# Optimization experiments

Hardware: AMD Instinct MI355X
Metric: run time of the kernel (lower is better)

Reference implementation:

```python
import jax, jax.numpy as jnp
import numpy as np

N = 100_000      # nodes
E = 1_600_000    # edges
D_IN = 256       # input feature dim
H, C = 4, 32     # heads, per-head channels (out_channels=32)
D_OUT = H * C    # 128
EPS = 1e-5


def setup_inputs() -> dict:
    key = jax.random.key(0)
    ks = jax.random.split(key, 8)
    f = jnp.float32
    return {
        "x": jax.random.normal(ks[0], (N, D_IN), f),
        "edge_index": jax.random.randint(ks[1], (2, E), 0, N, dtype=jnp.int32),
        "Wq": jax.random.normal(ks[2], (D_IN, D_OUT), f) * 0.05,
        "bq": jnp.zeros((D_OUT,), f),
        "Wk": jax.random.normal(ks[3], (D_IN, D_OUT), f) * 0.05,
        "bk": jnp.zeros((D_OUT,), f),
        "Wv": jax.random.normal(ks[4], (D_IN, D_OUT), f) * 0.05,
        "bv": jnp.zeros((D_OUT,), f),
        "Wskip": jax.random.normal(ks[5], (D_IN, D_OUT), f) * 0.05,
        "bskip": jnp.zeros((D_OUT,), f),
        "gn_weight": jnp.ones((D_OUT,), f),
        "gn_bias": jnp.zeros((D_OUT,), f),
        "gn_mean_scale": jnp.ones((D_OUT,), f),
    }


def reference(x, edge_index, Wq, bq, Wk, bk, Wv, bv, Wskip, bskip,
              gn_weight, gn_bias, gn_mean_scale):
    n = x.shape[0]
    src, dst = edge_index[0], edge_index[1]  # message flows src -> dst

    # ---- TransformerConv (heads=4, concat=True, root_weight=True) ----
    q = (x @ Wq + bq).reshape(n, H, C)
    k = (x @ Wk + bk).reshape(n, H, C)
    v = (x @ Wv + bv).reshape(n, H, C)

    # per-edge attention logits [E, H]
    score = jnp.einsum("ehc,ehc->eh", q[dst], k[src]) / jnp.sqrt(jnp.float32(C))

    # segment softmax over incoming edges of each destination node
    m = jax.ops.segment_max(score, dst, num_segments=n)        # [N, H]
    e = jnp.exp(score - m[dst])                                # [E, H]
    denom = jax.ops.segment_sum(e, dst, num_segments=n)        # [N, H]
    alpha = e / denom[dst]                                     # [E, H]

    # weighted aggregation of values: [E, H, C] -> [N, H, C]
    msg = alpha[:, :, None] * v[src]
    out = jax.ops.segment_sum(msg, dst, num_segments=n).reshape(n, D_OUT)

    # root (skip) transform
    out = out + x @ Wskip + bskip

    # ---- GraphNorm (single graph) ----
    mean = out.mean(axis=0)                                    # [D_OUT]
    centered = out - mean * gn_mean_scale
    var = (centered * centered).mean(axis=0)
    out = gn_weight * centered * jax.lax.rsqrt(var + EPS) + gn_bias

    # ---- Mish ----
    return out * jnp.tanh(jax.nn.softplus(out))
```

## Files before the change

### kernel.cpp

```cpp
#include <hip/hip_runtime.h>
#include <hip/hip_bf16.h>
#include <math.h>

#define N_NODES 100000
#define N_EDGES 1600000
#define D_IN    256
#define D_OUT   128
#define NHEAD   4
#define CH      32
#define GN_EPS  1e-5f

typedef __attribute__((ext_vector_type(8))) short bf16x8;
typedef __attribute__((ext_vector_type(4))) float f32x4;

__device__ inline float bf2f(unsigned short u) {
    return __uint_as_float(((unsigned int)u) << 16);
}
__device__ inline unsigned short f2bf(float f) {
    unsigned int x = __float_as_uint(f);
    unsigned int r = (x + 0x7fffu + ((x >> 16) & 1u)) >> 16;
    return (unsigned short)r;
}
__device__ inline unsigned int pk2bf(float a, float b) {
    __hip_bfloat162 h = __float22bfloat162_rn(float2{a, b});
    return *(unsigned int*)&h;
}
__device__ inline float mishf(float x) {
    if (x > 15.0f) return x;
    float ex = __expf(x);
    float t = ex * (ex + 2.0f);
    return x * t / (t + 2.0f);
}
__device__ inline void gload_lds16(const void* g, void* l) {
    __builtin_amdgcn_global_load_lds(
        (const __attribute__((address_space(1))) unsigned int*)g,
        (__attribute__((address_space(3))) unsigned int*)l,
        16, 0, 0);
}

__global__ void prep_w(const float* __restrict__ Wq, const float* __restrict__ Wk,
                       const float* __restrict__ Wv, const float* __restrict__ Wsk,
                       const float* __restrict__ bq, const float* __restrict__ bk,
                       const float* __restrict__ bv, const float* __restrict__ bsk,
                       unsigned short* __restrict__ Wt2, float* __restrict__ bcat) {
    int idx = blockIdx.x * 256 + threadIdx.x;
    int k   = idx >> 9;
    int col = idx & 511;
    int which = col >> 7, c = col & 127;
    const float* W = (which == 0) ? Wq : (which == 1) ? Wk : (which == 2) ? Wv : Wsk;
    int ks = k >> 5, cc = (k >> 3) & 3, j = k & 7;
    int p = cc ^ ((col >> 2) & 3);
    Wt2[(size_t)ks * 16384 + col * 32 + p * 8 + j] = f2bf(W[(size_t)k * 128 + c]);
    if (idx < 512) {
        int w2 = idx >> 7, c2 = idx & 127;
        const float* b = (w2 == 0) ? bq : (w2 == 1) ? bk : (w2 == 2) ? bv : bsk;
        bcat[idx] = b[c2];
    }
}

__global__ __launch_bounds__(512, 4) void gemm_mfma(
    const float* __restrict__ x, const unsigned short* __restrict__ Wt2,
    const float* __restrict__ bcat,
    unsigned short* __restrict__ qb, unsigned short* __restrict__ kb,
    unsigned short* __restrict__ vb, float* __restrict__ skip)
{
    __shared__ unsigned short as_[2][64 * 32];
    __shared__ unsigned short bs_[2][512 * 32];
    const int tid = threadIdx.x;
    const int nb = blockIdx.x * 64;

    const int wave = tid >> 6, lane = tid & 63;
    const int lm = lane & 15, lk = lane >> 4;
    const int wr = wave >> 2, wc = wave & 3;

    const int srow = tid >> 3;
    const int sk4  = (tid & 7) * 4;
    float4 areg;

    auto loadA = [&](int ks) {
        areg = make_float4(0.f, 0.f, 0.f, 0.f);
        int grow = nb + srow;
        if (grow < N_NODES)
            areg = *(const float4*)(x + (size_t)grow * D_IN + ks * 32 + sk4);
    };
    auto writeA = [&](int pb) {
        int cc = sk4 >> 3;
        int p = cc ^ ((srow >> 2) & 3);
        uint2 w;
        w.x = pk2bf(areg.x, areg.y);
        w.y = pk2bf(areg.z, areg.w);
        *(uint2*)(as_[pb] + srow * 32 + p * 8 + (sk4 & 7)) = w;
    };
    auto stageB = [&](int ks, int pb) {
        const unsigned short* g = Wt2 + (size_t)ks * 16384;
        #pragma unroll
        for (int it = 0; it < 4; ++it) {
            int u = it * 512 + tid;
            gload_lds16(g + u * 8, bs_[pb] + u * 8);
        }
    };

    f32x4 acc[2][8] = {};

    stageB(0, 0);
    loadA(0);
    writeA(0);
    __syncthreads();

    for (int ks = 0; ks < 8; ++ks) {
        const int pb = ks & 1;
        if (ks < 7) {
            stageB(ks + 1, pb ^ 1);
            loadA(ks + 1);
        }

        bf16x8 a[2], b[8];
        #pragma unroll
        for (int rf = 0; rf < 2; ++rf) {
            int row = wr * 32 + rf * 16 + lm;
            int p = lk ^ ((row >> 2) & 3);
            a[rf] = *(const bf16x8*)(as_[pb] + row * 32 + p * 8);
        }
        #pragma unroll
        for (int cf = 0; cf < 8; ++cf) {
            int col = wc * 128 + cf * 16 + lm;
            int p = lk ^ ((col >> 2) & 3);
            b[cf] = *(const bf16x8*)(bs_[pb] + col * 32 + p * 8);
        }
        #pragma unroll
        for (int cf = 0; cf < 8; ++cf) {
            acc[0][cf] = __builtin_amdgcn_mfma_f32_16x16x32_bf16(a[0], b[cf], acc[0][cf], 0, 0, 0);
            acc[1][cf] = __builtin_amdgcn_mfma_f32_16x16x32_bf16(a[1], b[cf], acc[1][cf], 0, 0, 0);
        }

        if (ks < 7) writeA(pb ^ 1);
        __syncthreads();
    }

    unsigned short* dstb = (wc == 0) ? qb : (wc == 1) ? kb : vb;
    const float* biasp = bcat + wc * 128;
    #pragma unroll
    for (int rf = 0; rf < 2; ++rf) {
        #pragma unroll
        for (int j = 0; j < 4; ++j) {
            const int r = nb + wr * 32 + rf * 16 + lk * 4 + j;
            if (r < N_NODES) {
                if (wc == 3) {
                    #pragma unroll
                    for (int cf = 0; cf < 8; ++cf) {
                        const int col = cf * 16 + lm;
                        skip[(size_t)r * D_OUT + col] = acc[rf][cf][j] + biasp[col];
                    }
                } else {
                    #pragma unroll
                    for (int cf = 0; cf < 8; ++cf) {
                        const int col = cf * 16 + lm;
                        dstb[(size_t)r * D_OUT + col] = f2bf(acc[rf][cf][j] + biasp[col]);
                    }
                }
            }
        }
    }
}

__global__ void hist_kernel(const int* __restrict__ dst, int* __restrict__ deg) {
    int e = blockIdx.x * 256 + threadIdx.x;
    if (e < N_EDGES) atomicAdd(&deg[dst[e]], 1);
}

__global__ __launch_bounds__(256) void scan1(const int* __restrict__ deg,
                                             int* __restrict__ off,
                                             int* __restrict__ bsum) {
    __shared__ int lds[256];
    int t = threadIdx.x;
    int base = blockIdx.x * 1024 + t * 4;
    int d0 = 0, d1 = 0, d2 = 0, d3 = 0;
    if (base + 3 < N_NODES) {
        int4 dd = *(const int4*)(deg + base);
        d0 = dd.x; d1 = dd.y; d2 = dd.z; d3 = dd.w;
    } else {
        if (base     < N_NODES) d0 = deg[base];
        if (base + 1 < N_NODES) d1 = deg[base + 1];
        if (base + 2 < N_NODES) d2 = deg[base + 2];
        if (base + 3 < N_NODES) d3 = deg[base + 3];
    }
    int s = d0 + d1 + d2 + d3;
    lds[t] = s;
    __syncthreads();
    for (int d = 1; d < 256; d <<= 1) {
        int u = (t >= d) ? lds[t - d] : 0;
        __syncthreads();
        lds[t] += u;
        __syncthreads();
    }
    int excl = lds[t] - s;
    if (base     < N_NODES) off[base]     = excl;
    if (base + 1 < N_NODES) off[base + 1] = excl + d0;
    if (base + 2 < N_NODES) off[base + 2] = excl + d0 + d1;
    if (base + 3 < N_NODES) off[base + 3] = excl + d0 + d1 + d2;
    if (t == 255) bsum[blockIdx.x] = lds[255];
}

__global__ void scan2(int* __restrict__ bsum) {
    __shared__ int lds[128];
    int t = threadIdx.x;
    int v = (t < 98) ? bsum[t] : 0;
    lds[t] = v;
    __syncthreads();
    for (int d = 1; d < 128; d <<= 1) {
        int u = (t >= d) ? lds[t - d] : 0;
        __syncthreads();
        lds[t] += u;
        __syncthreads();
    }
    if (t < 98) bsum[t] = lds[t] - v;
}

__global__ void scan3(int* __restrict__ off, int* __restrict__ cursor,
                      const int* __restrict__ bsum) {
    int add = bsum[blockIdx.x];
    int base = blockIdx.x * 1024 + threadIdx.x * 4;
    #pragma unroll
    for (int j = 0; j < 4; ++j) {
        int idx = base + j;
        if (idx < N_NODES) {
            int vv = off[idx] + add;
            off[idx] = vv;
            cursor[idx] = vv;
        }
    }
}

__global__ void scatter_kernel(const int* __restrict__ src, const int* __restrict__ dst,
                               int* __restrict__ cursor, int* __restrict__ ssrc) {
    int e = blockIdx.x * 256 + threadIdx.x;
    if (e < N_EDGES) {
        int d = dst[e];
        int p = atomicAdd(&cursor[d], 1);
        ssrc[p] = src[e];
    }
}

__global__ __launch_bounds__(256) void aggregate(
    const unsigned short* __restrict__ qb, const unsigned short* __restrict__ kb,
    const unsigned short* __restrict__ vb,
    const int* __restrict__ off, const int* __restrict__ endp,
    const int* __restrict__ ssrc, float* __restrict__ out)
{
    const int wave = threadIdx.x >> 6;
    const int lane = threadIdx.x & 63;
    const int n = blockIdx.x * 4 + wave;
    const int c0 = lane * 2;
    const float scale = 0.17677669529663687f;

    unsigned int qv = *(const unsigned int*)(qb + (size_t)n * D_OUT + c0);
    float q0 = bf2f((unsigned short)(qv & 0xffffu));
    float q1 = bf2f((unsigned short)(qv >> 16));

    const int s0 = off[n], s1 = endp[n];

    float m = -1e30f, den = 0.f, a0 = 0.f, a1 = 0.f;

    int i = s0;
    for (; i + 8 <= s1; i += 8) {
        int s[8]; unsigned int kw[8], vw[8]; float p[8], w[8];
        #pragma unroll
        for (int u = 0; u < 8; ++u) s[u] = ssrc[i + u];
        #pragma unroll
        for (int u = 0; u < 8; ++u) kw[u] = *(const unsigned int*)(kb + (size_t)s[u] * D_OUT + c0);
        #pragma unroll
        for (int u = 0; u < 8; ++u) vw[u] = *(const unsigned int*)(vb + (size_t)s[u] * D_OUT + c0);
        #pragma unroll
        for (int u = 0; u < 8; ++u)
            p[u] = q0 * bf2f((unsigned short)(kw[u] & 0xffffu)) + q1 * bf2f((unsigned short)(kw[u] >> 16));
        #pragma unroll
        for (int u = 0; u < 8; ++u) {
            p[u] += __shfl_xor(p[u], 1);
            p[u] += __shfl_xor(p[u], 2);
            p[u] += __shfl_xor(p[u], 4);
            p[u] += __shfl_xor(p[u], 8);
            p[u] *= scale;
        }
        float pm = fmaxf(fmaxf(fmaxf(p[0], p[1]), fmaxf(p[2], p[3])),
                         fmaxf(fmaxf(p[4], p[5]), fmaxf(p[6], p[7])));
        float newm = fmaxf(m, pm);
        float corr = __expf(m - newm);
        float dsum = 0.f, s0a = 0.f, s1a = 0.f;
        #pragma unroll
        for (int u = 0; u < 8; ++u) {
            w[u] = __expf(p[u] - newm);
            dsum += w[u];
            s0a += w[u] * bf2f((unsigned short)(vw[u] & 0xffffu));
            s1a += w[u] * bf2f((unsigned short)(vw[u] >> 16));
        }
        den = den * corr + dsum;
        a0  = a0 * corr + s0a;
        a1  = a1 * corr + s1a;
        m = newm;
    }
    for (; i + 4 <= s1; i += 4) {
        int s[4]; unsigned int kw[4], vw[4]; float p[4], w[4];
        #pragma unroll
        for (int u = 0; u < 4; ++u) s[u] = ssrc[i + u];
        #pragma unroll
        for (int u = 0; u < 4; ++u) kw[u] = *(const unsigned int*)(kb + (size_t)s[u] * D_OUT + c0);
        #pragma unroll
        for (int u = 0; u < 4; ++u) vw[u] = *(const unsigned int*)(vb + (size_t)s[u] * D_OUT + c0);
        #pragma unroll
        for (int u = 0; u < 4; ++u)
            p[u] = q0 * bf2f((unsigned short)(kw[u] & 0xffffu)) + q1 * bf2f((unsigned short)(kw[u] >> 16));
        #pragma unroll
        for (int u = 0; u < 4; ++u) {
            p[u] += __shfl_xor(p[u], 1);
            p[u] += __shfl_xor(p[u], 2);
            p[u] += __shfl_xor(p[u], 4);
            p[u] += __shfl_xor(p[u], 8);
            p[u] *= scale;
        }
        float pm = fmaxf(fmaxf(p[0], p[1]), fmaxf(p[2], p[3]));
        float newm = fmaxf(m, pm);
        float corr = __expf(m - newm);
        float dsum = 0.f, s0a = 0.f, s1a = 0.f;
        #pragma unroll
        for (int u = 0; u < 4; ++u) {
            w[u] = __expf(p[u] - newm);
            dsum += w[u];
            s0a += w[u] * bf2f((unsigned short)(vw[u] & 0xffffu));
            s1a += w[u] * bf2f((unsigned short)(vw[u] >> 16));
        }
        den = den * corr + dsum;
        a0  = a0 * corr + s0a;
        a1  = a1 * corr + s1a;
        m = newm;
    }
    for (; i < s1; ++i) {
        int s = ssrc[i];
        unsigned int kv = *(const unsigned int*)(kb + (size_t)s * D_OUT + c0);
        unsigned int vv = *(const unsigned int*)(vb + (size_t)s * D_OUT + c0);
        float p = q0 * bf2f((unsigned short)(kv & 0xffffu)) + q1 * bf2f((unsigned short)(kv >> 16));
        p += __shfl_xor(p, 1);
        p += __shfl_xor(p, 2);
        p += __shfl_xor(p, 4);
        p += __shfl_xor(p, 8);
        p *= scale;
        float newm = fmaxf(m, p);
        float corr = __expf(m - newm);
        float w = __expf(p - newm);
        den = den * corr + w;
        a0 = a0 * corr + w * bf2f((unsigned short)(vv & 0xffffu));
        a1 = a1 * corr + w * bf2f((unsigned short)(vv >> 16));
        m = newm;
    }

    float invd = (den > 0.f) ? 1.0f / den : 0.f;
    size_t o = (size_t)n * D_OUT + c0;
    float2 sk = *(float2*)(out + o);
    sk.x += a0 * invd;
    sk.y += a1 * invd;
    *(float2*)(out + o) = sk;
}

__global__ __launch_bounds__(256) void norm_reduce(const float* __restrict__ out,
                                                   float* __restrict__ sums) {
    const int total = N_NODES * D_OUT;
    const int stride = gridDim.x * 256;
    int t = threadIdx.x;
    float s = 0.f, s2 = 0.f;
    for (int i = blockIdx.x * 256 + t; i < total; i += stride) {
        float v = out[i];
        s += v; s2 += v * v;
    }
    __shared__ float ls[256], lq[256];
    ls[t] = s; lq[t] = s2;
    __syncthreads();
    if (t < 128) {
        s  = ls[t] + ls[t + 128];
        s2 = lq[t] + lq[t + 128];
        atomicAdd(&sums[t], s);
        atomicAdd(&sums[128 + t], s2);
    }
}

__global__ void finalize(const float* __restrict__ sums, const float* __restrict__ gw,
                         const float* __restrict__ gb, const float* __restrict__ gms,
                         float* __restrict__ AB) {
    int c = threadIdx.x;
    const float invN = 1.0f / (float)N_NODES;
    float mean = sums[c] * invN;
    float ex2  = sums[128 + c] * invN;
    float mu = mean * gms[c];
    float var = ex2 - 2.f * mu * mean + mu * mu;
    float inv = rsqrtf(var + GN_EPS);
    float A = gw[c] * inv;
    AB[c] = A;
    AB[128 + c] = gb[c] - mu * A;
}

__global__ __launch_bounds__(256) void mish_kernel(float* __restrict__ out,
                                                   const float* __restrict__ AB) {
    int i = blockIdx.x * 256 + threadIdx.x;
    int c4 = (i << 2) & 127;
    float4 a  = *(const float4*)(AB + c4);
    float4 b  = *(const float4*)(AB + 128 + c4);
    float4 v  = *(float4*)(out + (size_t)i * 4);
    v.x = mishf(a.x * v.x + b.x);
    v.y = mishf(a.y * v.y + b.y);
    v.z = mishf(a.z * v.z + b.z);
    v.w = mishf(a.w * v.w + b.w);
    *(float4*)(out + (size_t)i * 4) = v;
}

extern "C" void kernel_launch(void* const* d_in, const int* in_sizes, int n_in,
                              void* d_out, int out_size, void* d_ws, size_t ws_size,
                              hipStream_t stream) {
    (void)in_sizes; (void)n_in; (void)out_size; (void)ws_size;

    const float* x    = (const float*)d_in[0];
    const int*   ei   = (const int*)d_in[1];
    const float* Wq   = (const float*)d_in[2];
    const float* bq   = (const float*)d_in[3];
    const float* Wk   = (const float*)d_in[4];
    const float* bk   = (const float*)d_in[5];
    const float* Wv   = (const float*)d_in[6];
    const float* bv   = (const float*)d_in[7];
    const float* Wsk  = (const float*)d_in[8];
    const float* bsk  = (const float*)d_in[9];
    const float* gw   = (const float*)d_in[10];
    const float* gb   = (const float*)d_in[11];
    const float* gms  = (const float*)d_in[12];
    float* out = (float*)d_out;

    char* ws = (char*)d_ws;
    size_t o = 0;
    auto alloc = [&](size_t bytes) -> char* {
        char* p = ws + o;
        o += (bytes + 255) & ~(size_t)255;
        return p;
    };

    unsigned short* qb = (unsigned short*)alloc((size_t)N_NODES * D_OUT * 2);
    unsigned short* kb = (unsigned short*)alloc((size_t)N_NODES * D_OUT * 2);
    unsigned short* vb = (unsigned short*)alloc((size_t)N_NODES * D_OUT * 2);
    int* ssrc     = (int*)alloc((size_t)N_EDGES * 4);
    int* deg      = (int*)alloc((size_t)N_NODES * 4);
    int* off      = (int*)alloc((size_t)(N_NODES + 1) * 4);
    int* cursor   = (int*)alloc((size_t)N_NODES * 4);
    int* bsum     = (int*)alloc(512);
    float* sums   = (float*)alloc(1024);
    float* AB     = (float*)alloc(1024);
    unsigned short* Wt2 = (unsigned short*)alloc((size_t)512 * 256 * 2);
    float* bcat   = (float*)alloc(512 * 4);

    const int* srcp = ei;
    const int* dstp = ei + N_EDGES;

    hipMemsetAsync(deg, 0, (size_t)N_NODES * 4, stream);
    hipMemsetAsync(sums, 0, 256 * 4, stream);

    prep_w<<<512, 256, 0, stream>>>(Wq, Wk, Wv, Wsk, bq, bk, bv, bsk, Wt2, bcat);
    gemm_mfma<<<(N_NODES + 63) / 64, 512, 0, stream>>>(x, Wt2, bcat, qb, kb, vb, out);

    hist_kernel<<<(N_EDGES + 255) / 256, 256, 0, stream>>>(dstp, deg);
    scan1<<<98, 256, 0, stream>>>(deg, off, bsum);
    scan2<<<1, 128, 0, stream>>>(bsum);
    scan3<<<98, 256, 0, stream>>>(off, cursor, bsum);
    scatter_kernel<<<(N_EDGES + 255) / 256, 256, 0, stream>>>(srcp, dstp, cursor, ssrc);

    aggregate<<<N_NODES / 4, 256, 0, stream>>>(qb, kb, vb, off, cursor, ssrc, out);

    norm_reduce<<<512, 256, 0, stream>>>(out, sums);
    finalize<<<1, 128, 0, stream>>>(sums, gw, gb, gms, AB);
    mish_kernel<<<(N_NODES * D_OUT / 4) / 256, 256, 0, stream>>>(out, AB);
}
```

Baseline: 447.4 us.

## Two-pass bucketed CSR build and split edges across 4 lane groups in aggregate

Replaces the per-edge global atomic scatter with a two-level bucket sort: edges are first grouped into 512-node buckets using block-local counts and one global atomic per bucket, then each bucket's edges are placed using LDS atomics. This is meant to cut contention and random global atomics when building the CSR, at the cost of an extra 8-byte-per-edge temporary pass. The aggregate kernel now has each wave handle four edges at a time, one per 16-lane group, each lane covering 8 channels with 16-byte loads. The four partial online softmaxes are merged with cross-group shuffles at the end. This gives more memory parallelism and shorter reductions, but uses more registers.

```diff
diff --git a/kernel.cpp b/kernel.cpp
--- a/kernel.cpp
+++ b/kernel.cpp
@@ -9,6 +9,10 @@
 #define NHEAD   4
 #define CH      32
 #define GN_EPS  1e-5f
+
+#define BSHIFT  9
+#define BNODES  512
+#define NBUCK   196
 
 typedef __attribute__((ext_vector_type(8))) short bf16x8;
 typedef __attribute__((ext_vector_type(4))) float f32x4;
@@ -216,148 +220,150 @@
     if (t < 98) bsum[t] = lds[t] - v;
 }
 
-__global__ void scan3(int* __restrict__ off, int* __restrict__ cursor,
-                      const int* __restrict__ bsum) {
+__global__ void scan3(int* __restrict__ off, const int* __restrict__ bsum) {
     int add = bsum[blockIdx.x];
     int base = blockIdx.x * 1024 + threadIdx.x * 4;
     #pragma unroll
     for (int j = 0; j < 4; ++j) {
         int idx = base + j;
-        if (idx < N_NODES) {
-            int vv = off[idx] + add;
-            off[idx] = vv;
-            cursor[idx] = vv;
-        }
-    }
-}
-
-__global__ void scatter_kernel(const int* __restrict__ src, const int* __restrict__ dst,
-                               int* __restrict__ cursor, int* __restrict__ ssrc) {
-    int e = blockIdx.x * 256 + threadIdx.x;
-    if (e < N_EDGES) {
-        int d = dst[e];
-        int p = atomicAdd(&cursor[d], 1);
-        ssrc[p] = src[e];
+        if (idx < N_NODES) off[idx] += add;
+    }
+}
+
+__global__ void binit(const int* __restrict__ off, int* __restrict__ bcur) {
+    int t = threadIdx.x;
+    if (t < NBUCK) bcur[t] = off[t * BNODES];
+}
+
+__global__ __launch_bounds__(256) void bucket1(const int* __restrict__ src,
+                                               const int* __restrict__ dst,
+                                               int* __restrict__ bcur,
+                                               int2* __restrict__ tpair) {
+    __shared__ int cnt[NBUCK], base[NBUCK], cnt2[NBUCK];
+    const int t = threadIdx.x;
+    const int e0 = blockIdx.x * 4096;
+    if (t < NBUCK) { cnt[t] = 0; cnt2[t] = 0; }
+    __syncthreads();
+
+    #pragma unroll
+    for (int u = 0; u < 16; ++u) {
+        int e = e0 + u * 256 + t;
+        if (e < N_EDGES) atomicAdd(&cnt[dst[e] >> BSHIFT], 1);
+    }
+    __syncthreads();
+    if (t < NBUCK && cnt[t] > 0) base[t] = atomicAdd(&bcur[t], cnt[t]);
+    __syncthreads();
+
+    #pragma unroll
+    for (int u = 0; u < 16; ++u) {
+        int e = e0 + u * 256 + t;
+        if (e < N_EDGES) {
+            int d = dst[e];
+            int b = d >> BSHIFT;
+            int idx = atomicAdd(&cnt2[b], 1);
+            tpair[base[b] + idx] = make_int2(src[e], d);
+        }
+    }
+}
+
+__global__ __launch_bounds__(256) void bucket2(const int* __restrict__ off,
+                                               const int2* __restrict__ tpair,
+                                               int* __restrict__ ssrc) {
+    __shared__ int cur[BNODES];
+    const int b = blockIdx.x;
+    const int t = threadIdx.x;
+    const int n0 = b * BNODES;
+    #pragma unroll
+    for (int u = 0; u < 2; ++u) {
+        int idx = n0 + u * 256 + t;
+        cur[u * 256 + t] = (idx < N_NODES) ? off[idx] : 0;
+    }
+    __syncthreads();
+
+    const int start = off[n0];
+    const int end = (b == NBUCK - 1) ? N_EDGES : off[n0 + BNODES];
+    for (int i = start + t; i < end; i += 256) {
+        int2 pr = tpair[i];
+        int q = atomicAdd(&cur[pr.y - n0], 1);
+        ssrc[q] = pr.x;
     }
 }
 
 __global__ __launch_bounds__(256) void aggregate(
     const unsigned short* __restrict__ qb, const unsigned short* __restrict__ kb,
     const unsigned short* __restrict__ vb,
-    const int* __restrict__ off, const int* __restrict__ endp,
+    const int* __restrict__ off, const int* __restrict__ deg,
     const int* __restrict__ ssrc, float* __restrict__ out)
 {
     const int wave = threadIdx.x >> 6;
     const int lane = threadIdx.x & 63;
     const int n = blockIdx.x * 4 + wave;
-    const int c0 = lane * 2;
+    const int grp = lane >> 4, sl = lane & 15;
+    const int cbase = sl * 8;
     const float scale = 0.17677669529663687f;
 
-    unsigned int qv = *(const unsigned int*)(qb + (size_t)n * D_OUT + c0);
-    float q0 = bf2f((unsigned short)(qv & 0xffffu));
-    float q1 = bf2f((unsigned short)(qv >> 16));
-
-    const int s0 = off[n], s1 = endp[n];
-
-    float m = -1e30f, den = 0.f, a0 = 0.f, a1 = 0.f;
-
-    int i = s0;
-    for (; i + 8 <= s1; i += 8) {
-        int s[8]; unsigned int kw[8], vw[8]; float p[8], w[8];
-        #pragma unroll
-        for (int u = 0; u < 8; ++u) s[u] = ssrc[i + u];
-        #pragma unroll
-        for (int u = 0; u < 8; ++u) kw[u] = *(const unsigned int*)(kb + (size_t)s[u] * D_OUT + c0);
-        #pragma unroll
-        for (int u = 0; u < 8; ++u) vw[u] = *(const unsigned int*)(vb + (size_t)s[u] * D_OUT + c0);
-        #pragma unroll
-        for (int u = 0; u < 8; ++u)
-            p[u] = q0 * bf2f((unsigned short)(kw[u] & 0xffffu)) + q1 * bf2f((unsigned short)(kw[u] >> 16));
-        #pragma unroll
-        for (int u = 0; u < 8; ++u) {
-            p[u] += __shfl_xor(p[u], 1);
-            p[u] += __shfl_xor(p[u], 2);
-            p[u] += __shfl_xor(p[u], 4);
-            p[u] += __shfl_xor(p[u], 8);
-            p[u] *= scale;
-        }
-        float pm = fmaxf(fmaxf(fmaxf(p[0], p[1]), fmaxf(p[2], p[3])),
-                         fmaxf(fmaxf(p[4], p[5]), fmaxf(p[6], p[7])));
-        float newm = fmaxf(m, pm);
-        float corr = __expf(m - newm);
-        float dsum = 0.f, s0a = 0.f, s1a = 0.f;
-        #pragma unroll
-        for (int u = 0; u < 8; ++u) {
-            w[u] = __expf(p[u] - newm);
-            dsum += w[u];
-            s0a += w[u] * bf2f((unsigned short)(vw[u] & 0xffffu));
-            s1a += w[u] * bf2f((unsigned short)(vw[u] >> 16));
-        }
-        den = den * corr + dsum;
-        a0  = a0 * corr + s0a;
-        a1  = a1 * corr + s1a;
-        m = newm;
-    }
-    for (; i + 4 <= s1; i += 4) {
-        int s[4]; unsigned int kw[4], vw[4]; float p[4], w[4];
-        #pragma unroll
-        for (int u = 0; u < 4; ++u) s[u] = ssrc[i + u];
-        #pragma unroll
-        for (int u = 0; u < 4; ++u) kw[u] = *(const unsigned int*)(kb + (size_t)s[u] * D_OUT + c0);
-        #pragma unroll
-        for (int u = 0; u < 4; ++u) vw[u] = *(const unsigned int*)(vb + (size_t)s[u] * D_OUT + c0);
-        #pragma unroll
-        for (int u = 0; u < 4; ++u)
-            p[u] = q0 * bf2f((unsigned short)(kw[u] & 0xffffu)) + q1 * bf2f((unsigned short)(kw[u] >> 16));
-        #pragma unroll
-        for (int u = 0; u < 4; ++u) {
-            p[u] += __shfl_xor(p[u], 1);
-            p[u] += __shfl_xor(p[u], 2);
-            p[u] += __shfl_xor(p[u], 4);
-            p[u] += __shfl_xor(p[u], 8);
-            p[u] *= scale;
-        }
-        float pm = fmaxf(fmaxf(p[0], p[1]), fmaxf(p[2], p[3]));
-        float newm = fmaxf(m, pm);
-        float corr = __expf(m - newm);
-        float dsum = 0.f, s0a = 0.f, s1a = 0.f;
-        #pragma unroll
-        for (int u = 0; u < 4; ++u) {
-            w[u] = __expf(p[u] - newm);
-            dsum += w[u];
-            s0a += w[u] * bf2f((unsigned short)(vw[u] & 0xffffu));
-            s1a += w[u] * bf2f((unsigned short)(vw[u] >> 16));
-        }
-        den = den * corr + dsum;
-        a0  = a0 * corr + s0a;
-        a1  = a1 * corr + s1a;
-        m = newm;
-    }
-    for (; i < s1; ++i) {
+    bf16x8 q8 = *(const bf16x8*)(qb + (size_t)n * D_OUT + cbase);
+    float qf[8];
+    #pragma unroll
+    for (int j = 0; j < 8; ++j) qf[j] = bf2f((unsigned short)q8[j]);
+
+    const int s0 = off[n];
+    const int s1 = s0 + deg[n];
+
+    float m = -1e30f, den = 0.f;
+    float acc[8] = {0.f, 0.f, 0.f, 0.f, 0.f, 0.f, 0.f, 0.f};
+
+    auto edge = [&](int i) {
         int s = ssrc[i];
-        unsigned int kv = *(const unsigned int*)(kb + (size_t)s * D_OUT + c0);
-        unsigned int vv = *(const unsigned int*)(vb + (size_t)s * D_OUT + c0);
-        float p = q0 * bf2f((unsigned short)(kv & 0xffffu)) + q1 * bf2f((unsigned short)(kv >> 16));
-        p += __shfl_xor(p, 1);
-        p += __shfl_xor(p, 2);
-        p += __shfl_xor(p, 4);
-        p += __shfl_xor(p, 8);
-        p *= scale;
+        bf16x8 k8 = *(const bf16x8*)(kb + (size_t)s * D_OUT + cbase);
+        bf16x8 v8 = *(const bf16x8*)(vb + (size_t)s * D_OUT + cbase);
+        float part = 0.f;
+        #pragma unroll
+        for (int j = 0; j < 8; ++j) part += qf[j] * bf2f((unsigned short)k8[j]);
+        part += __shfl_xor(part, 1);
+        part += __shfl_xor(part, 2);
+        float p = part * scale;
         float newm = fmaxf(m, p);
         float corr = __expf(m - newm);
         float w = __expf(p - newm);
         den = den * corr + w;
-        a0 = a0 * corr + w * bf2f((unsigned short)(vv & 0xffffu));
-        a1 = a1 * corr + w * bf2f((unsigned short)(vv >> 16));
+        #pragma unroll
+        for (int j = 0; j < 8; ++j)
+            acc[j] = acc[j] * corr + w * bf2f((unsigned short)v8[j]);
         m = newm;
-    }
-
-    float invd = (den > 0.f) ? 1.0f / den : 0.f;
-    size_t o = (size_t)n * D_OUT + c0;
-    float2 sk = *(float2*)(out + o);
-    sk.x += a0 * invd;
-    sk.y += a1 * invd;
-    *(float2*)(out + o) = sk;
+    };
+
+    int i = s0 + grp;
+    for (; i + 4 < s1; i += 8) { edge(i); edge(i + 4); }
+    if (i < s1) edge(i);
+
+    #pragma unroll
+    for (int d = 16; d <= 32; d <<= 1) {
+        float mo = __shfl_xor(m, d);
+        float deno = __shfl_xor(den, d);
+        float M = fmaxf(m, mo);
+        float c1 = __expf(m - M), c2 = __expf(mo - M);
+        den = den * c1 + deno * c2;
+        #pragma unroll
+        for (int j = 0; j < 8; ++j) {
+            float ao = __shfl_xor(acc[j], d);
+            acc[j] = acc[j] * c1 + ao * c2;
+        }
+        m = M;
+    }
+
+    if (grp == 0) {
+        float invd = (den > 0.f) ? 1.0f / den : 0.f;
+        size_t o = (size_t)n * D_OUT + cbase;
+        float4 o0 = *(float4*)(out + o);
+        float4 o1 = *(float4*)(out + o + 4);
+        o0.x += acc[0] * invd; o0.y += acc[1] * invd;
+        o0.z += acc[2] * invd; o0.w += acc[3] * invd;
+        o1.x += acc[4] * invd; o1.y += acc[5] * invd;
+        o1.z += acc[6] * invd; o1.w += acc[7] * invd;
+        *(float4*)(out + o) = o0;
+        *(float4*)(out + o + 4) = o1;
+    }
 }
 
 __global__ __launch_bounds__(256) void norm_reduce(const float* __restrict__ out,
@@ -442,9 +448,10 @@
     unsigned short* kb = (unsigned short*)alloc((size_t)N_NODES * D_OUT * 2);
     unsigned short* vb = (unsigned short*)alloc((size_t)N_NODES * D_OUT * 2);
     int* ssrc     = (int*)alloc((size_t)N_EDGES * 4);
+    int2* tpair   = (int2*)alloc((size_t)N_EDGES * 8);
     int* deg      = (int*)alloc((size_t)N_NODES * 4);
     int* off      = (int*)alloc((size_t)(N_NODES + 1) * 4);
-    int* cursor   = (int*)alloc((size_t)N_NODES * 4);
+    int* bcur     = (int*)alloc(1024);
     int* bsum     = (int*)alloc(512);
     float* sums   = (float*)alloc(1024);
     float* AB     = (float*)alloc(1024);
@@ -463,10 +470,13 @@
     hist_kernel<<<(N_EDGES + 255) / 256, 256, 0, stream>>>(dstp, deg);
     scan1<<<98, 256, 0, stream>>>(deg, off, bsum);
     scan2<<<1, 128, 0, stream>>>(bsum);
-    scan3<<<98, 256, 0, stream>>>(off, cursor, bsum);
-    scatter_kernel<<<(N_EDGES + 255) / 256, 256, 0, stream>>>(srcp, dstp, cursor, ssrc);
-
-    aggregate<<<N_NODES / 4, 256, 0, stream>>>(qb, kb, vb, off, cursor, ssrc, out);
+    scan3<<<98, 256, 0, stream>>>(off, bsum);
+
+    binit<<<1, 256, 0, stream>>>(off, bcur);
+    bucket1<<<(N_EDGES + 4095) / 4096, 256, 0, stream>>>(srcp, dstp, bcur, tpair);
+    bucket2<<<NBUCK, 256, 0, stream>>>(off, tpair, ssrc);
+
+    aggregate<<<N_NODES / 4, 256, 0, stream>>>(qb, kb, vb, off, deg, ssrc, out);
 
     norm_reduce<<<512, 256, 0, stream>>>(out, sums);
     finalize<<<1, 128, 0, stream>>>(sums, gw, gb, gms, AB);
```

Result: faster. 364.1 us (-18.6%).
